# Optimization experiments

Measured on AMD Instinct MI355X. Metric: run time of the kernel, lower is better.

## Reference

```python
import jax, jax.numpy as jnp
import numpy as np

NEG_SLOPE = 0.2
LN_EPS = 1e-5


def gat_conv(x, src, dst, n_nodes, W, a_src, a_dst, b, concat):
    # W: [F_in, H*C]; a_src, a_dst: [H, C]; b: [H*C] if concat else [C]
    H, C = a_src.shape
    h = (x @ W).reshape(-1, H, C)                      # [N, H, C]
    # per-node attention scores, gathered per edge
    s_src = jnp.einsum('nhc,hc->nh', h, a_src)          # [N, H]
    s_dst = jnp.einsum('nhc,hc->nh', h, a_dst)          # [N, H]
    e = jax.nn.leaky_relu(s_src[src] + s_dst[dst], NEG_SLOPE)  # [E, H]
    # segment softmax over incoming edges of each dst node
    e_max = jax.ops.segment_max(e, dst, num_segments=n_nodes)  # [N, H]
    w = jnp.exp(e - e_max[dst])
    denom = jax.ops.segment_sum(w, dst, num_segments=n_nodes)
    alpha = w / (denom[dst] + 1e-16)                    # [E, H]
    # weighted scatter-aggregate of source messages
    msg = h[src] * alpha[:, :, None]                    # [E, H, C]
    out = jax.ops.segment_sum(msg, dst, num_segments=n_nodes)  # [N, H, C]
    out = out.reshape(n_nodes, H * C) if concat else out.mean(axis=1)
    return out + b


def layer_norm(x, g, b):
    mu = x.mean(-1, keepdims=True)
    var = ((x - mu) ** 2).mean(-1, keepdims=True)
    return (x - mu) * jax.lax.rsqrt(var + LN_EPS) * g + b


def setup_inputs() -> dict:
    key = jax.random.key(0)
    ks = jax.random.split(key, 16)
    N, E, F_in = 50000, 400000, 128
    H1, C1 = 4, 128          # conv1: heads=4, hidden=128, concat -> 512
    C2 = 64                  # conv2: heads=1, out=64
    sd = lambda fan: 1.0 / np.sqrt(fan)
    inp = {
        'x': jax.random.normal(ks[0], (N, F_in), jnp.float32),
        'edge_index': jax.random.randint(ks[1], (2, E), 0, N, jnp.int64),
        'num_nodes': N,
        'W1': jax.random.normal(ks[2], (F_in, H1 * C1), jnp.float32) * sd(F_in),
        'a_src1': jax.random.normal(ks[3], (H1, C1), jnp.float32) * sd(C1),
        'a_dst1': jax.random.normal(ks[4], (H1, C1), jnp.float32) * sd(C1),
        'b1': jnp.zeros((H1 * C1,), jnp.float32),
        'W2': jax.random.normal(ks[5], (H1 * C1, C2), jnp.float32) * sd(H1 * C1),
        'a_src2': jax.random.normal(ks[6], (1, C2), jnp.float32) * sd(C2),
        'a_dst2': jax.random.normal(ks[7], (1, C2), jnp.float32) * sd(C2),
        'b2': jnp.zeros((C2,), jnp.float32),
        'Wm1': jax.random.normal(ks[8], (C2, 32), jnp.float32) * sd(C2),
        'bm1': jnp.zeros((32,), jnp.float32),
        'g_ln': jnp.ones((32,), jnp.float32),
        'b_ln': jnp.zeros((32,), jnp.float32),
        'Wm2': jax.random.normal(ks[9], (32, 16), jnp.float32) * sd(32),
        'bm2': jnp.zeros((16,), jnp.float32),
    }
    return inp


def reference(x, edge_index, num_nodes, W1, a_src1, a_dst1, b1, W2, a_src2, a_dst2, b2, Wm1, bm1, g_ln, b_ln, Wm2, bm2):
    N = num_nodes
    # PyG GATConv add_self_loops=True
    loop = jnp.arange(N, dtype=edge_index.dtype)
    src = jnp.concatenate([edge_index[0], loop])
    dst = jnp.concatenate([edge_index[1], loop])
    # dropout layers are identity in eval mode
    h = jax.nn.elu(gat_conv(x, src, dst, N, W1, a_src1, a_dst1, b1, concat=True))
    h = jax.nn.elu(gat_conv(h, src, dst, N, W2, a_src2, a_dst2, b2, concat=False))
    h = jax.nn.relu(layer_norm(h @ Wm1 + bm1, g_ln, b_ln))
    return h @ Wm2 + bm2  # [N, 2*n_spectral_dims]
```

## Files before the change

### kernel.cpp

```cpp
#include <hip/hip_runtime.h>
#include <cmath>


#define F_IN 128
#define H1   4
#define C1   128
#define D1   512
#define C2   64
#define DM1  32
#define DM2  16

#define LRELU(x) ((x) > 0.f ? (x) : 0.2f * (x))

typedef float f32x4 __attribute__((ext_vector_type(4)));
typedef short short8 __attribute__((ext_vector_type(8)));

static __device__ __forceinline__ float bf2f(unsigned short u) {
    return __builtin_bit_cast(float, (unsigned)u << 16);
}
static __device__ __forceinline__ unsigned short f2bf(float f) {
    unsigned u = __builtin_bit_cast(unsigned, f);
    u = (u + 0x7fffu + ((u >> 16) & 1u)) >> 16;
    return (unsigned short)u;
}
static __device__ __forceinline__ float bflo(unsigned d) {
    return __builtin_bit_cast(float, d << 16);
}
static __device__ __forceinline__ float bfhi(unsigned d) {
    return __builtin_bit_cast(float, d & 0xffff0000u);
}

__global__ void k_detect(const void* ei, int E, int* flag) {
    __shared__ int any;
    if (threadIdx.x == 0) any = 0;
    __syncthreads();
    const int* p = (const int*)ei;
    int cnt = E < 4096 ? E : 4096;
    int stride = E / cnt;
    int local = 0;
    for (int i = threadIdx.x; i < cnt; i += blockDim.x) {
        long long idx = (long long)i * stride;
        local |= p[2 * idx + 1];
    }
    if (local) atomicOr(&any, 1);
    __syncthreads();
    if (threadIdx.x == 0) *flag = (any == 0) ? 1 : 0;
}

__global__ void k_convert_prep(const void* ei, const int* flag, int E, int N,
                               int* src32, int* dst32, int* deg,
                               const float* __restrict__ x,
                               const float* __restrict__ W1,
                               const float* __restrict__ W2,
                               unsigned short* __restrict__ xb,
                               unsigned short* __restrict__ W1t,
                               unsigned short* __restrict__ W2t, int n8) {
    int i = blockIdx.x * blockDim.x + threadIdx.x;
    int Etot = E + N;
    if (i < Etot) {
        int s, d;
        if (i < E) {
            if (*flag) {
                const long long* q = (const long long*)ei;
                s = (int)q[i];
                d = (int)q[(size_t)E + i];
            } else {
                const int* q = (const int*)ei;
                s = q[i];
                d = q[(size_t)E + i];
            }
        } else {
            s = i - E;
            d = i - E;
        }
        src32[i] = s;
        dst32[i] = d;
        atomicAdd(&deg[d], 1);
        return;
    }
    int i1 = i - Etot;
    if (i1 < n8) {
        const float4* p = (const float4*)(x + (size_t)i1 * 8);
        float4 a = p[0], b = p[1];
        unsigned short r[8] = {f2bf(a.x), f2bf(a.y), f2bf(a.z), f2bf(a.w),
                               f2bf(b.x), f2bf(b.y), f2bf(b.z), f2bf(b.w)};
        *(short8*)(xb + (size_t)i1 * 8) = *(const short8*)r;
        return;
    }
    int i2 = i1 - n8;
    if (i2 < F_IN * D1) {
        int nn = i2 / F_IN, kk = i2 - nn * F_IN;
        W1t[i2] = f2bf(W1[(size_t)kk * D1 + nn]);
        return;
    }
    int i3 = i2 - F_IN * D1;
    if (i3 < D1 * C2) {
        int nn = i3 / D1, kk = i3 - nn * D1;
        W2t[i3] = f2bf(W2[(size_t)kk * C2 + nn]);
    }
}

__global__ __launch_bounds__(256) void k_scan1(const int* __restrict__ deg,
                                               int* __restrict__ bsum, int N) {
    int t = threadIdx.x;
    int base = blockIdx.x * 1024 + t * 4;
    int s = 0;
    if (base + 3 < N) {
        int4 v = *(const int4*)&deg[base];
        s = v.x + v.y + v.z + v.w;
    } else {
        for (int k = 0; k < 4; k++)
            if (base + k < N) s += deg[base + k];
    }
#pragma unroll
    for (int o = 1; o < 64; o <<= 1) s += __shfl_xor(s, o, 64);
    __shared__ int ws[4];
    if ((t & 63) == 0) ws[t >> 6] = s;
    __syncthreads();
    if (t == 0) bsum[blockIdx.x] = ws[0] + ws[1] + ws[2] + ws[3];
}

__global__ __launch_bounds__(1024) void k_scan2(const int* __restrict__ bsum,
                                                int* __restrict__ boff, int nb) {
    __shared__ int wsum[16];
    __shared__ int woff[16];
    int t = threadIdx.x, lane = t & 63, wid = t >> 6;
    int v = (t < nb) ? bsum[t] : 0;
    int x = v;
#pragma unroll
    for (int o = 1; o < 64; o <<= 1) {
        int tv = __shfl_up(x, o, 64);
        if (lane >= o) x += tv;
    }
    if (lane == 63) wsum[wid] = x;
    __syncthreads();
    if (wid == 0) {
        int y = (lane < 16) ? wsum[lane] : 0;
        int z = y;
#pragma unroll
        for (int o = 1; o < 16; o <<= 1) {
            int tv = __shfl_up(z, o, 64);
            if (lane >= o) z += tv;
        }
        if (lane < 16) woff[lane] = z - y;
    }
    __syncthreads();
    if (t < nb) boff[t] = woff[wid] + x - v;
}

__global__ __launch_bounds__(256) void k_scan3(const int* __restrict__ deg,
                                               const int* __restrict__ boff,
                                               int* __restrict__ rowstart,
                                               int* __restrict__ cursor, int N,
                                               int Etot) {
    int t = threadIdx.x, lane = t & 63, wid = t >> 6;
    int base = blockIdx.x * 1024 + t * 4;
    int v0 = 0, v1 = 0, v2 = 0, v3 = 0;
    if (base + 3 < N) {
        int4 v = *(const int4*)&deg[base];
        v0 = v.x; v1 = v.y; v2 = v.z; v3 = v.w;
    } else {
        if (base + 0 < N) v0 = deg[base + 0];
        if (base + 1 < N) v1 = deg[base + 1];
        if (base + 2 < N) v2 = deg[base + 2];
        if (base + 3 < N) v3 = deg[base + 3];
    }
    int s4 = v0 + v1 + v2 + v3;
    int x = s4;
#pragma unroll
    for (int o = 1; o < 64; o <<= 1) {
        int tv = __shfl_up(x, o, 64);
        if (lane >= o) x += tv;
    }
    __shared__ int ws[4];
    if (lane == 63) ws[wid] = x;
    __syncthreads();
    int woff = 0;
#pragma unroll
    for (int w = 0; w < 4; w++)
        if (w < wid) woff += ws[w];
    int ex = boff[blockIdx.x] + woff + (x - s4);
    int e0 = ex, e1 = ex + v0, e2 = e1 + v1, e3 = e2 + v2;
    if (base + 0 < N) { rowstart[base + 0] = e0; cursor[base + 0] = e0; }
    if (base + 1 < N) { rowstart[base + 1] = e1; cursor[base + 1] = e1; }
    if (base + 2 < N) { rowstart[base + 2] = e2; cursor[base + 2] = e2; }
    if (base + 3 < N) { rowstart[base + 3] = e3; cursor[base + 3] = e3; }
    if (blockIdx.x == 0 && t == 0) rowstart[N] = Etot;
}

__global__ void k_fill(const int* __restrict__ src32, const int* __restrict__ dst32,
                       int* __restrict__ cursor, int* __restrict__ adj, int Etot) {
    int i = blockIdx.x * blockDim.x + threadIdx.x;
    if (i < Etot) {
        int d = dst32[i];
        int pos = atomicAdd(&cursor[d], 1);
        adj[pos] = src32[i];
    }
}

template <int WM, int WN, int MF, int NF, bool OUT_BF16, int SC_MODE>
__global__ __launch_bounds__(256) void k_gemm_bf16(
    const unsigned short* __restrict__ A, const unsigned short* __restrict__ Bt,
    void* __restrict__ C, int M, int K, int NC,
    const float* __restrict__ avs, const float* __restrict__ avd,
    float* __restrict__ s_src, float* __restrict__ s_dst) {
    constexpr int BM = WM * MF * 16;
    constexpr int BN = WN * NF * 16;
    constexpr int BK = 64;
    __shared__ unsigned short As[BM * BK];
    __shared__ unsigned short Bs[BN * BK];
    __shared__ float ps_lds[WN][BM], pd_lds[WN][BM];
    const int tid = threadIdx.x;
    const int row0 = blockIdx.x * BM, col0 = blockIdx.y * BN;
    const int wave = tid >> 6, lane = tid & 63;
    const int wr = wave / WN, wc = wave % WN;
    const int lrow = lane & 15, lkg = lane >> 4;
    f32x4 acc[MF][NF] = {};
    for (int k0 = 0; k0 < K; k0 += BK) {
#pragma unroll
        for (int inst = 0; inst < (BM * 8) / 256; ++inst) {
            int ibase = inst * 256 + wave * 64;
            int i = ibase + lane;
            int r = i >> 3, u = i & 7, su = u ^ (r & 7);
            const unsigned short* gp = A + (size_t)(row0 + r) * K + k0 + su * 8;
            __builtin_amdgcn_global_load_lds(
                (const __attribute__((address_space(1))) void*)gp,
                (__attribute__((address_space(3))) void*)&As[ibase * 8], 16, 0, 0);
        }
#pragma unroll
        for (int inst = 0; inst < (BN * 8) / 256; ++inst) {
            int ibase = inst * 256 + wave * 64;
            int i = ibase + lane;
            int r = i >> 3, u = i & 7, su = u ^ (r & 7);
            const unsigned short* gp = Bt + (size_t)(col0 + r) * K + k0 + su * 8;
            __builtin_amdgcn_global_load_lds(
                (const __attribute__((address_space(1))) void*)gp,
                (__attribute__((address_space(3))) void*)&Bs[ibase * 8], 16, 0, 0);
        }
        __syncthreads();
#pragma unroll
        for (int kk = 0; kk < BK; kk += 32) {
            short8 af[MF], bfr[NF];
#pragma unroll
            for (int m = 0; m < MF; m++) {
                int ar = wr * MF * 16 + m * 16 + lrow;
                int au = kk / 8 + lkg;
                af[m] = *(const short8*)&As[(ar * 8 + (au ^ (lrow & 7))) * 8];
            }
#pragma unroll
            for (int n = 0; n < NF; n++) {
                int br = wc * NF * 16 + n * 16 + lrow;
                int au = kk / 8 + lkg;
                bfr[n] = *(const short8*)&Bs[(br * 8 + (au ^ (lrow & 7))) * 8];
            }
#pragma unroll
            for (int m = 0; m < MF; m++)
#pragma unroll
                for (int n = 0; n < NF; n++)
                    acc[m][n] = __builtin_amdgcn_mfma_f32_16x16x32_bf16(
                        af[m], bfr[n], acc[m][n], 0, 0, 0);
        }
        __syncthreads();
    }
#pragma unroll
    for (int m = 0; m < MF; m++)
#pragma unroll
        for (int n = 0; n < NF; n++)
#pragma unroll
            for (int r = 0; r < 4; r++) {
                int gr = row0 + wr * MF * 16 + m * 16 + lkg * 4 + r;
                int gc = col0 + wc * NF * 16 + n * 16 + lrow;
                if (gr < M) {
                    if (OUT_BF16)
                        ((unsigned short*)C)[(size_t)gr * NC + gc] = f2bf(acc[m][n][r]);
                    else
                        ((float*)C)[(size_t)gr * NC + gc] = acc[m][n][r];
                }
            }
    if (SC_MODE) {
        float asv[NF], adv[NF];
#pragma unroll
        for (int n = 0; n < NF; n++) {
            int gc = col0 + wc * NF * 16 + n * 16 + lrow;
            asv[n] = avs[gc];
            adv[n] = avd[gc];
        }
#pragma unroll
        for (int m = 0; m < MF; m++)
#pragma unroll
            for (int r = 0; r < 4; r++) {
                float ps = 0.f, pd = 0.f;
#pragma unroll
                for (int n = 0; n < NF; n++) {
                    ps += acc[m][n][r] * asv[n];
                    pd += acc[m][n][r] * adv[n];
                }
#pragma unroll
                for (int o = 1; o < 16; o <<= 1) {
                    ps += __shfl_xor(ps, o, 64);
                    pd += __shfl_xor(pd, o, 64);
                }
                if (lrow == 0) {
                    int lr = wr * MF * 16 + m * 16 + lkg * 4 + r;
                    ps_lds[wc][lr] = ps;
                    pd_lds[wc][lr] = pd;
                }
            }
        __syncthreads();
        for (int rr = tid; rr < BM; rr += 256) {
            int gr = row0 + rr;
            if (gr < M) {
                float s = 0.f, d = 0.f;
#pragma unroll
                for (int w = 0; w < WN; w++) {
                    s += ps_lds[w][rr];
                    d += pd_lds[w][rr];
                }
                if (SC_MODE == 1) {
                    s_src[(size_t)gr * H1 + blockIdx.y] = s;
                    s_dst[(size_t)gr * H1 + blockIdx.y] = d;
                } else {
                    s_src[gr] = s;
                    s_dst[gr] = d;
                }
            }
        }
    }
}

__global__ __launch_bounds__(256) void k_agg1(
    const unsigned short* __restrict__ h1b, const float* __restrict__ s_src,
    const float* __restrict__ s_dst, const int* __restrict__ rowstart,
    const int* __restrict__ adj, const float* __restrict__ b1,
    unsigned short* __restrict__ out1, int N) {
    int wv = (blockIdx.x * blockDim.x + threadIdx.x) >> 6;
    if (wv >= N) return;
    int lane = threadIdx.x & 63;
    int beg = rowstart[wv], end = rowstart[wv + 1];
    int h4 = lane & 3, jj = lane >> 2;
    float sdh = s_dst[(size_t)wv * 4 + h4];
    float m = -1e30f;
    for (int c0 = beg; c0 < end; c0 += 16) {
        int j = c0 + jj;
        if (j < end) {
            int sj = adj[j];
            float e = LRELU(s_src[(size_t)sj * 4 + h4] + sdh);
            m = fmaxf(m, e);
        }
    }
#pragma unroll
    for (int o = 4; o < 64; o <<= 1) m = fmaxf(m, __shfl_xor(m, o, 64));
    float dn = 0.f;
    for (int c0 = beg; c0 < end; c0 += 16) {
        int j = c0 + jj;
        if (j < end) {
            int sj = adj[j];
            float e = LRELU(s_src[(size_t)sj * 4 + h4] + sdh);
            dn += __expf(e - m);
        }
    }
#pragma unroll
    for (int o = 4; o < 64; o <<= 1) dn += __shfl_xor(dn, o, 64);
    float inv = 1.f / (dn + 1e-16f);
    int hg = lane >> 4;
    float aL[4] = {}, aH[4] = {};
#define ACC1(vv, aa)                                   \
    do {                                               \
        aL[0] += (aa)*bflo(vv.x); aH[0] += (aa)*bfhi(vv.x); \
        aL[1] += (aa)*bflo(vv.y); aH[1] += (aa)*bfhi(vv.y); \
        aL[2] += (aa)*bflo(vv.z); aH[2] += (aa)*bfhi(vv.z); \
        aL[3] += (aa)*bflo(vv.w); aH[3] += (aa)*bfhi(vv.w); \
    } while (0)
    for (int c0 = beg; c0 < end; c0 += 16) {
        int j = c0 + jj;
        float av = 0.f;
        int sjv = 0;
        if (j < end) {
            sjv = adj[j];
            float e = LRELU(s_src[(size_t)sjv * 4 + h4] + sdh);
            av = __expf(e - m) * inv;
        }
        int cnt = min(16, end - c0);
        int j2 = 0;
        for (; j2 + 4 <= cnt; j2 += 4) {
            int l0 = (j2 + 0) * 4 + hg, l1 = (j2 + 1) * 4 + hg;
            int l2 = (j2 + 2) * 4 + hg, l3 = (j2 + 3) * 4 + hg;
            int s0 = __shfl(sjv, l0, 64), s1 = __shfl(sjv, l1, 64);
            int s2 = __shfl(sjv, l2, 64), s3 = __shfl(sjv, l3, 64);
            float a0 = __shfl(av, l0, 64), a1 = __shfl(av, l1, 64);
            float a2 = __shfl(av, l2, 64), a3 = __shfl(av, l3, 64);
            uint4 v0 = *(const uint4*)&h1b[(size_t)s0 * D1 + lane * 8];
            uint4 v1 = *(const uint4*)&h1b[(size_t)s1 * D1 + lane * 8];
            uint4 v2 = *(const uint4*)&h1b[(size_t)s2 * D1 + lane * 8];
            uint4 v3 = *(const uint4*)&h1b[(size_t)s3 * D1 + lane * 8];
            ACC1(v0, a0); ACC1(v1, a1); ACC1(v2, a2); ACC1(v3, a3);
        }
        for (; j2 < cnt; ++j2) {
            int l0 = j2 * 4 + hg;
            int s0 = __shfl(sjv, l0, 64);
            float a0 = __shfl(av, l0, 64);
            uint4 v0 = *(const uint4*)&h1b[(size_t)s0 * D1 + lane * 8];
            ACC1(v0, a0);
        }
    }
#undef ACC1
    const float4* bp = (const float4*)&b1[lane * 8];
    float4 bb0 = bp[0], bb1 = bp[1];
    float r[8];
    r[0] = aL[0] + bb0.x; r[1] = aH[0] + bb0.y;
    r[2] = aL[1] + bb0.z; r[3] = aH[1] + bb0.w;
    r[4] = aL[2] + bb1.x; r[5] = aH[2] + bb1.y;
    r[6] = aL[3] + bb1.z; r[7] = aH[3] + bb1.w;
    unsigned short o16[8];
#pragma unroll
    for (int i = 0; i < 8; i++) {
        float z = r[i] > 0.f ? r[i] : expm1f(r[i]);
        o16[i] = f2bf(z);
    }
    *(short8*)&out1[(size_t)wv * D1 + lane * 8] = *(const short8*)o16;
}

__global__ __launch_bounds__(256) void k_agg2(
    const unsigned short* __restrict__ h2lin, const float* __restrict__ s_src,
    const float* __restrict__ s_dst, const int* __restrict__ rowstart,
    const int* __restrict__ adj, const float* __restrict__ b2,
    float* __restrict__ h2, int N) {
    int wv = (blockIdx.x * blockDim.x + threadIdx.x) >> 6;
    if (wv >= N) return;
    int lane = threadIdx.x & 63;
    int beg = rowstart[wv], end = rowstart[wv + 1];
    float sd = s_dst[wv];
    float m = -1e30f;
    for (int c0 = beg; c0 < end; c0 += 64) {
        int j = c0 + lane;
        if (j < end) m = fmaxf(m, LRELU(s_src[adj[j]] + sd));
    }
#pragma unroll
    for (int o = 1; o < 64; o <<= 1) m = fmaxf(m, __shfl_xor(m, o, 64));
    float dn = 0.f;
    for (int c0 = beg; c0 < end; c0 += 64) {
        int j = c0 + lane;
        if (j < end) dn += __expf(LRELU(s_src[adj[j]] + sd) - m);
    }
#pragma unroll
    for (int o = 1; o < 64; o <<= 1) dn += __shfl_xor(dn, o, 64);
    float inv = 1.f / (dn + 1e-16f);
    int eg = lane >> 4, ch = (lane & 15) * 4;
    float a0 = 0.f, a1 = 0.f, a2 = 0.f, a3 = 0.f;
    for (int j0 = beg; j0 < end; j0 += 4) {
        int j = j0 + eg;
        if (j < end) {
            int sj = adj[j];
            float a = __expf(LRELU(s_src[sj] + sd) - m) * inv;
            uint2 rv = *(const uint2*)&h2lin[(size_t)sj * C2 + ch];
            a0 += a * bflo(rv.x); a1 += a * bfhi(rv.x);
            a2 += a * bflo(rv.y); a3 += a * bfhi(rv.y);
        }
    }
#pragma unroll
    for (int o = 16; o < 64; o <<= 1) {
        a0 += __shfl_xor(a0, o, 64);
        a1 += __shfl_xor(a1, o, 64);
        a2 += __shfl_xor(a2, o, 64);
        a3 += __shfl_xor(a3, o, 64);
    }
    if (lane < 16) {
        const float4 bb = *(const float4*)&b2[ch];
        float r0 = a0 + bb.x, r1 = a1 + bb.y, r2 = a2 + bb.z, r3 = a3 + bb.w;
        r0 = r0 > 0.f ? r0 : expm1f(r0);
        r1 = r1 > 0.f ? r1 : expm1f(r1);
        r2 = r2 > 0.f ? r2 : expm1f(r2);
        r3 = r3 > 0.f ? r3 : expm1f(r3);
        *(float4*)&h2[(size_t)wv * C2 + ch] = make_float4(r0, r1, r2, r3);
    }
}

__global__ __launch_bounds__(256) void k_mlp(
    const float* __restrict__ h2, const float* __restrict__ Wm1,
    const float* __restrict__ bm1, const float* __restrict__ g_ln,
    const float* __restrict__ b_ln, const float* __restrict__ Wm2,
    const float* __restrict__ bm2, float* __restrict__ out, int N) {
    __shared__ float w1[C2 * DM1];
    __shared__ float w2[DM1 * DM2];
    __shared__ float cb1[DM1], cg[DM1], cbl[DM1], cb2[DM2];
    int tid = threadIdx.x;
    for (int i = tid; i < C2 * DM1; i += 256) w1[i] = Wm1[i];
    for (int i = tid; i < DM1 * DM2; i += 256) w2[i] = Wm2[i];
    if (tid < DM1) {
        cb1[tid] = bm1[tid];
        cg[tid] = g_ln[tid];
        cbl[tid] = b_ln[tid];
    } else if (tid < DM1 + DM2) {
        cb2[tid - DM1] = bm2[tid - DM1];
    }
    __syncthreads();
    int n = blockIdx.x * 256 + tid;
    if (n >= N) return;
    float h[C2];
    const float4* hp = (const float4*)&h2[(size_t)n * C2];
#pragma unroll
    for (int i = 0; i < C2 / 4; i++) {
        float4 v = hp[i];
        h[4 * i] = v.x; h[4 * i + 1] = v.y;
        h[4 * i + 2] = v.z; h[4 * i + 3] = v.w;
    }
    float t[DM1];
#pragma unroll
    for (int j = 0; j < DM1; j++) {
        float a = cb1[j];
#pragma unroll
        for (int c = 0; c < C2; c++) a += h[c] * w1[c * DM1 + j];
        t[j] = a;
    }
    float mu = 0.f;
#pragma unroll
    for (int j = 0; j < DM1; j++) mu += t[j];
    mu *= (1.f / DM1);
    float var = 0.f;
#pragma unroll
    for (int j = 0; j < DM1; j++) {
        float d = t[j] - mu;
        var += d * d;
    }
    var *= (1.f / DM1);
    float rs = rsqrtf(var + 1e-5f);
#pragma unroll
    for (int j = 0; j < DM1; j++) {
        float z = (t[j] - mu) * rs * cg[j] + cbl[j];
        t[j] = z > 0.f ? z : 0.f;
    }
    float o[DM2];
#pragma unroll
    for (int k = 0; k < DM2; k++) {
        float a = cb2[k];
#pragma unroll
        for (int j = 0; j < DM1; j++) a += t[j] * w2[j * DM2 + k];
        o[k] = a;
    }
    float4* op = (float4*)&out[(size_t)n * DM2];
    op[0] = make_float4(o[0], o[1], o[2], o[3]);
    op[1] = make_float4(o[4], o[5], o[6], o[7]);
    op[2] = make_float4(o[8], o[9], o[10], o[11]);
    op[3] = make_float4(o[12], o[13], o[14], o[15]);
}

extern "C" void kernel_launch(void* const* d_in, const int* in_sizes, int n_in,
                              void* d_out, int out_size, void* d_ws,
                              size_t ws_size, hipStream_t stream) {
    const float* x      = (const float*)d_in[0];
    const void*  ei     = d_in[1];
    const float* W1     = (const float*)d_in[3];
    const float* a_src1 = (const float*)d_in[4];
    const float* a_dst1 = (const float*)d_in[5];
    const float* b1     = (const float*)d_in[6];
    const float* W2     = (const float*)d_in[7];
    const float* a_src2 = (const float*)d_in[8];
    const float* a_dst2 = (const float*)d_in[9];
    const float* b2     = (const float*)d_in[10];
    const float* Wm1    = (const float*)d_in[11];
    const float* bm1    = (const float*)d_in[12];
    const float* g_ln   = (const float*)d_in[13];
    const float* b_ln   = (const float*)d_in[14];
    const float* Wm2    = (const float*)d_in[15];
    const float* bm2    = (const float*)d_in[16];

    const int N    = in_sizes[0] / F_IN;
    const int E    = in_sizes[1] / 2;
    const int Etot = E + N;
    const int nb   = (N + 1023) / 1024;

    char* ws = (char*)d_ws;
    size_t off = 0;
    auto alloc = [&](size_t bytes) {
        size_t o = off;
        off += (bytes + 255) & ~(size_t)255;
        return o;
    };
    int*   flag     = (int*)(ws + alloc(4));
    int*   src32    = (int*)(ws + alloc((size_t)Etot * 4));
    int*   dst32    = (int*)(ws + alloc((size_t)Etot * 4));
    int*   deg      = (int*)(ws + alloc((size_t)N * 4));
    int*   bsum     = (int*)(ws + alloc(4096 * 4));
    int*   boff     = (int*)(ws + alloc(4096 * 4));
    int*   rowstart = (int*)(ws + alloc((size_t)(N + 1) * 4));
    int*   cursor   = (int*)(ws + alloc((size_t)N * 4));
    int*   adj      = (int*)(ws + alloc((size_t)Etot * 4));
    float* s_src1   = (float*)(ws + alloc((size_t)N * H1 * 4));
    float* s_dst1   = (float*)(ws + alloc((size_t)N * H1 * 4));
    unsigned short* xb    = (unsigned short*)(ws + alloc((size_t)N * F_IN * 2));
    unsigned short* W1t   = (unsigned short*)(ws + alloc((size_t)F_IN * D1 * 2));
    unsigned short* W2t   = (unsigned short*)(ws + alloc((size_t)D1 * C2 * 2));
    unsigned short* h1b   = (unsigned short*)(ws + alloc((size_t)N * D1 * 2));
    unsigned short* out1  = (unsigned short*)(ws + alloc((size_t)N * D1 * 2));
    unsigned short* h2lin = (unsigned short*)(ws + alloc((size_t)N * C2 * 2));
    float* h2    = (float*)(ws + alloc((size_t)N * C2 * 4));
    float* s_src2 = s_src1;
    float* s_dst2 = s_dst1;

    hipMemsetAsync(deg, 0, (size_t)N * 4, stream);
    k_detect<<<1, 256, 0, stream>>>(ei, E, flag);
    int n8 = N * F_IN / 8;
    int total_cp = Etot + n8 + F_IN * D1 + D1 * C2;
    k_convert_prep<<<(total_cp + 255) / 256, 256, 0, stream>>>(
        ei, flag, E, N, src32, dst32, deg, x, W1, W2, xb, W1t, W2t, n8);
    k_scan1<<<nb, 256, 0, stream>>>(deg, bsum, N);
    k_scan2<<<1, 1024, 0, stream>>>(bsum, boff, nb);
    k_scan3<<<nb, 256, 0, stream>>>(deg, boff, rowstart, cursor, N, Etot);
    k_fill<<<(Etot + 255) / 256, 256, 0, stream>>>(src32, dst32, cursor, adj, Etot);

    k_gemm_bf16<2, 2, 4, 4, true, 1>
        <<<dim3((N + 127) / 128, D1 / 128), 256, 0, stream>>>(
            xb, W1t, h1b, N, F_IN, D1, a_src1, a_dst1, s_src1, s_dst1);
    k_agg1<<<(N * 64 + 255) / 256, 256, 0, stream>>>(h1b, s_src1, s_dst1, rowstart,
                                                     adj, b1, out1, N);

    k_gemm_bf16<4, 1, 2, 4, true, 2>
        <<<dim3((N + 127) / 128, 1), 256, 0, stream>>>(
            out1, W2t, h2lin, N, D1, C2, a_src2, a_dst2, s_src2, s_dst2);
    k_agg2<<<(N * 64 + 255) / 256, 256, 0, stream>>>(h2lin, s_src2, s_dst2, rowstart,
                                                     adj, b2, h2, N);

    k_mlp<<<(N + 255) / 256, 256, 0, stream>>>(h2, Wm1, bm1, g_ln, b_ln, Wm2, bm2,
                                               (float*)d_out, N);
}
```

Baseline: 340.9 us.

## Use atomic ranks for CSR fill, online softmax in aggregations, LDS edge broadcast

CSR construction now records each edge's atomic rank during degree counting, so the fill pass needs no second atomic pass over a cursor array. Both aggregation kernels fuse the max and denominator passes into one online-softmax pass, and agg1 reuses the first chunk's scores. agg1 broadcasts source indices and weights through LDS instead of many shuffles. The second GEMM switches to a smaller 64-row tile to launch more blocks, at the cost of an extra rank array and more exp calls in the online update.

```diff
diff --git a/kernel.cpp b/kernel.cpp
--- a/kernel.cpp
+++ b/kernel.cpp
@@ -48,7 +48,7 @@
 }
 
 __global__ void k_convert_prep(const void* ei, const int* flag, int E, int N,
-                               int* src32, int* dst32, int* deg,
+                               int* src32, int* dst32, int* deg, int* rank32,
                                const float* __restrict__ x,
                                const float* __restrict__ W1,
                                const float* __restrict__ W2,
@@ -75,7 +75,7 @@
         }
         src32[i] = s;
         dst32[i] = d;
-        atomicAdd(&deg[d], 1);
+        rank32[i] = atomicAdd(&deg[d], 1);
         return;
     }
     int i1 = i - Etot;
@@ -150,8 +150,7 @@
 
 __global__ __launch_bounds__(256) void k_scan3(const int* __restrict__ deg,
                                                const int* __restrict__ boff,
-                                               int* __restrict__ rowstart,
-                                               int* __restrict__ cursor, int N,
+                                               int* __restrict__ rowstart, int N,
                                                int Etot) {
     int t = threadIdx.x, lane = t & 63, wid = t >> 6;
     int base = blockIdx.x * 1024 + t * 4;
@@ -181,21 +180,19 @@
         if (w < wid) woff += ws[w];
     int ex = boff[blockIdx.x] + woff + (x - s4);
     int e0 = ex, e1 = ex + v0, e2 = e1 + v1, e3 = e2 + v2;
-    if (base + 0 < N) { rowstart[base + 0] = e0; cursor[base + 0] = e0; }
-    if (base + 1 < N) { rowstart[base + 1] = e1; cursor[base + 1] = e1; }
-    if (base + 2 < N) { rowstart[base + 2] = e2; cursor[base + 2] = e2; }
-    if (base + 3 < N) { rowstart[base + 3] = e3; cursor[base + 3] = e3; }
+    if (base + 0 < N) rowstart[base + 0] = e0;
+    if (base + 1 < N) rowstart[base + 1] = e1;
+    if (base + 2 < N) rowstart[base + 2] = e2;
+    if (base + 3 < N) rowstart[base + 3] = e3;
     if (blockIdx.x == 0 && t == 0) rowstart[N] = Etot;
 }
 
 __global__ void k_fill(const int* __restrict__ src32, const int* __restrict__ dst32,
-                       int* __restrict__ cursor, int* __restrict__ adj, int Etot) {
+                       const int* __restrict__ rank32,
+                       const int* __restrict__ rowstart, int* __restrict__ adj,
+                       int Etot) {
     int i = blockIdx.x * blockDim.x + threadIdx.x;
-    if (i < Etot) {
-        int d = dst32[i];
-        int pos = atomicAdd(&cursor[d], 1);
-        adj[pos] = src32[i];
-    }
+    if (i < Etot) adj[rowstart[dst32[i]] + rank32[i]] = src32[i];
 }
 
 template <int WM, int WN, int MF, int NF, bool OUT_BF16, int SC_MODE>
@@ -333,73 +330,88 @@
     const float* __restrict__ s_dst, const int* __restrict__ rowstart,
     const int* __restrict__ adj, const float* __restrict__ b1,
     unsigned short* __restrict__ out1, int N) {
+    __shared__ uint2 ex_lds[4][64];
     int wv = (blockIdx.x * blockDim.x + threadIdx.x) >> 6;
     if (wv >= N) return;
+    int wv4 = (threadIdx.x >> 6) & 3;
     int lane = threadIdx.x & 63;
     int beg = rowstart[wv], end = rowstart[wv + 1];
     int h4 = lane & 3, jj = lane >> 2;
     float sdh = s_dst[(size_t)wv * 4 + h4];
-    float m = -1e30f;
-    for (int c0 = beg; c0 < end; c0 += 16) {
-        int j = c0 + jj;
+    int nch = (end - beg + 15) >> 4;
+    float e0st = -1e30f;
+    int s0st = 0;
+    float m = -1e30f, dn = 0.f;
+    for (int c = 0; c < nch; ++c) {
+        int j = beg + c * 16 + jj;
+        float e = -1e30f;
+        int sj = 0;
         if (j < end) {
-            int sj = adj[j];
-            float e = LRELU(s_src[(size_t)sj * 4 + h4] + sdh);
-            m = fmaxf(m, e);
-        }
-    }
-#pragma unroll
-    for (int o = 4; o < 64; o <<= 1) m = fmaxf(m, __shfl_xor(m, o, 64));
-    float dn = 0.f;
-    for (int c0 = beg; c0 < end; c0 += 16) {
-        int j = c0 + jj;
-        if (j < end) {
-            int sj = adj[j];
-            float e = LRELU(s_src[(size_t)sj * 4 + h4] + sdh);
-            dn += __expf(e - m);
-        }
-    }
-#pragma unroll
-    for (int o = 4; o < 64; o <<= 1) dn += __shfl_xor(dn, o, 64);
+            sj = adj[j];
+            e = LRELU(s_src[(size_t)sj * 4 + h4] + sdh);
+        }
+        if (c == 0) { e0st = e; s0st = sj; }
+        float nm = fmaxf(m, e);
+        dn = dn * __expf(m - nm) + ((j < end) ? __expf(e - nm) : 0.f);
+        m = nm;
+    }
+#pragma unroll
+    for (int o = 4; o < 64; o <<= 1) {
+        float om = __shfl_xor(m, o, 64);
+        float od = __shfl_xor(dn, o, 64);
+        float nm = fmaxf(m, om);
+        dn = dn * __expf(m - nm) + od * __expf(om - nm);
+        m = nm;
+    }
     float inv = 1.f / (dn + 1e-16f);
     int hg = lane >> 4;
     float aL[4] = {}, aH[4] = {};
-#define ACC1(vv, aa)                                   \
-    do {                                               \
+#define ACC1(vv, aa)                                        \
+    do {                                                    \
         aL[0] += (aa)*bflo(vv.x); aH[0] += (aa)*bfhi(vv.x); \
         aL[1] += (aa)*bflo(vv.y); aH[1] += (aa)*bfhi(vv.y); \
         aL[2] += (aa)*bflo(vv.z); aH[2] += (aa)*bfhi(vv.z); \
         aL[3] += (aa)*bflo(vv.w); aH[3] += (aa)*bfhi(vv.w); \
     } while (0)
-    for (int c0 = beg; c0 < end; c0 += 16) {
-        int j = c0 + jj;
-        float av = 0.f;
-        int sjv = 0;
-        if (j < end) {
-            sjv = adj[j];
-            float e = LRELU(s_src[(size_t)sjv * 4 + h4] + sdh);
-            av = __expf(e - m) * inv;
-        }
-        int cnt = min(16, end - c0);
+    for (int c = 0; c < nch; ++c) {
+        int j = beg + c * 16 + jj;
+        float e;
+        int sj;
+        if (c == 0) {
+            e = e0st;
+            sj = s0st;
+        } else {
+            sj = 0;
+            e = -1e30f;
+            if (j < end) {
+                sj = adj[j];
+                e = LRELU(s_src[(size_t)sj * 4 + h4] + sdh);
+            }
+        }
+        float av = (j < end) ? __expf(e - m) * inv : 0.f;
+        ex_lds[wv4][lane] = make_uint2((unsigned)sj, __builtin_bit_cast(unsigned, av));
+        asm volatile("s_waitcnt lgkmcnt(0)" ::: "memory");
+        int cnt = min(16, end - beg - c * 16);
         int j2 = 0;
         for (; j2 + 4 <= cnt; j2 += 4) {
-            int l0 = (j2 + 0) * 4 + hg, l1 = (j2 + 1) * 4 + hg;
-            int l2 = (j2 + 2) * 4 + hg, l3 = (j2 + 3) * 4 + hg;
-            int s0 = __shfl(sjv, l0, 64), s1 = __shfl(sjv, l1, 64);
-            int s2 = __shfl(sjv, l2, 64), s3 = __shfl(sjv, l3, 64);
-            float a0 = __shfl(av, l0, 64), a1 = __shfl(av, l1, 64);
-            float a2 = __shfl(av, l2, 64), a3 = __shfl(av, l3, 64);
-            uint4 v0 = *(const uint4*)&h1b[(size_t)s0 * D1 + lane * 8];
-            uint4 v1 = *(const uint4*)&h1b[(size_t)s1 * D1 + lane * 8];
-            uint4 v2 = *(const uint4*)&h1b[(size_t)s2 * D1 + lane * 8];
-            uint4 v3 = *(const uint4*)&h1b[(size_t)s3 * D1 + lane * 8];
+            uint2 e0 = ex_lds[wv4][(j2 + 0) * 4 + hg];
+            uint2 e1 = ex_lds[wv4][(j2 + 1) * 4 + hg];
+            uint2 e2 = ex_lds[wv4][(j2 + 2) * 4 + hg];
+            uint2 e3 = ex_lds[wv4][(j2 + 3) * 4 + hg];
+            uint4 v0 = *(const uint4*)&h1b[(size_t)e0.x * D1 + lane * 8];
+            uint4 v1 = *(const uint4*)&h1b[(size_t)e1.x * D1 + lane * 8];
+            uint4 v2 = *(const uint4*)&h1b[(size_t)e2.x * D1 + lane * 8];
+            uint4 v3 = *(const uint4*)&h1b[(size_t)e3.x * D1 + lane * 8];
+            float a0 = __builtin_bit_cast(float, e0.y);
+            float a1 = __builtin_bit_cast(float, e1.y);
+            float a2 = __builtin_bit_cast(float, e2.y);
+            float a3 = __builtin_bit_cast(float, e3.y);
             ACC1(v0, a0); ACC1(v1, a1); ACC1(v2, a2); ACC1(v3, a3);
         }
         for (; j2 < cnt; ++j2) {
-            int l0 = j2 * 4 + hg;
-            int s0 = __shfl(sjv, l0, 64);
-            float a0 = __shfl(av, l0, 64);
-            uint4 v0 = *(const uint4*)&h1b[(size_t)s0 * D1 + lane * 8];
+            uint2 e0 = ex_lds[wv4][j2 * 4 + hg];
+            uint4 v0 = *(const uint4*)&h1b[(size_t)e0.x * D1 + lane * 8];
+            float a0 = __builtin_bit_cast(float, e0.y);
             ACC1(v0, a0);
         }
     }
@@ -430,20 +442,23 @@
     int lane = threadIdx.x & 63;
     int beg = rowstart[wv], end = rowstart[wv + 1];
     float sd = s_dst[wv];
-    float m = -1e30f;
+    float m = -1e30f, dn = 0.f;
     for (int c0 = beg; c0 < end; c0 += 64) {
         int j = c0 + lane;
-        if (j < end) m = fmaxf(m, LRELU(s_src[adj[j]] + sd));
-    }
-#pragma unroll
-    for (int o = 1; o < 64; o <<= 1) m = fmaxf(m, __shfl_xor(m, o, 64));
-    float dn = 0.f;
-    for (int c0 = beg; c0 < end; c0 += 64) {
-        int j = c0 + lane;
-        if (j < end) dn += __expf(LRELU(s_src[adj[j]] + sd) - m);
-    }
-#pragma unroll
-    for (int o = 1; o < 64; o <<= 1) dn += __shfl_xor(dn, o, 64);
+        float e = -1e30f;
+        if (j < end) e = LRELU(s_src[adj[j]] + sd);
+        float nm = fmaxf(m, e);
+        dn = dn * __expf(m - nm) + ((j < end) ? __expf(e - nm) : 0.f);
+        m = nm;
+    }
+#pragma unroll
+    for (int o = 1; o < 64; o <<= 1) {
+        float om = __shfl_xor(m, o, 64);
+        float od = __shfl_xor(dn, o, 64);
+        float nm = fmaxf(m, om);
+        dn = dn * __expf(m - nm) + od * __expf(om - nm);
+        m = nm;
+    }
     float inv = 1.f / (dn + 1e-16f);
     int eg = lane >> 4, ch = (lane & 15) * 4;
     float a0 = 0.f, a1 = 0.f, a2 = 0.f, a3 = 0.f;
@@ -579,11 +594,11 @@
     int*   flag     = (int*)(ws + alloc(4));
     int*   src32    = (int*)(ws + alloc((size_t)Etot * 4));
     int*   dst32    = (int*)(ws + alloc((size_t)Etot * 4));
+    int*   rank32   = (int*)(ws + alloc((size_t)Etot * 4));
     int*   deg      = (int*)(ws + alloc((size_t)N * 4));
     int*   bsum     = (int*)(ws + alloc(4096 * 4));
     int*   boff     = (int*)(ws + alloc(4096 * 4));
     int*   rowstart = (int*)(ws + alloc((size_t)(N + 1) * 4));
-    int*   cursor   = (int*)(ws + alloc((size_t)N * 4));
     int*   adj      = (int*)(ws + alloc((size_t)Etot * 4));
     float* s_src1   = (float*)(ws + alloc((size_t)N * H1 * 4));
     float* s_dst1   = (float*)(ws + alloc((size_t)N * H1 * 4));
@@ -602,11 +617,12 @@
     int n8 = N * F_IN / 8;
     int total_cp = Etot + n8 + F_IN * D1 + D1 * C2;
     k_convert_prep<<<(total_cp + 255) / 256, 256, 0, stream>>>(
-        ei, flag, E, N, src32, dst32, deg, x, W1, W2, xb, W1t, W2t, n8);
+        ei, flag, E, N, src32, dst32, deg, rank32, x, W1, W2, xb, W1t, W2t, n8);
     k_scan1<<<nb, 256, 0, stream>>>(deg, bsum, N);
     k_scan2<<<1, 1024, 0, stream>>>(bsum, boff, nb);
-    k_scan3<<<nb, 256, 0, stream>>>(deg, boff, rowstart, cursor, N, Etot);
-    k_fill<<<(Etot + 255) / 256, 256, 0, stream>>>(src32, dst32, cursor, adj, Etot);
+    k_scan3<<<nb, 256, 0, stream>>>(deg, boff, rowstart, N, Etot);
+    k_fill<<<(Etot + 255) / 256, 256, 0, stream>>>(src32, dst32, rank32, rowstart,
+                                                   adj, Etot);
 
     k_gemm_bf16<2, 2, 4, 4, true, 1>
         <<<dim3((N + 127) / 128, D1 / 128), 256, 0, stream>>>(
@@ -614,8 +630,8 @@
     k_agg1<<<(N * 64 + 255) / 256, 256, 0, stream>>>(h1b, s_src1, s_dst1, rowstart,
                                                      adj, b1, out1, N);
 
-    k_gemm_bf16<4, 1, 2, 4, true, 2>
-        <<<dim3((N + 127) / 128, 1), 256, 0, stream>>>(
+    k_gemm_bf16<2, 2, 2, 2, true, 2>
+        <<<dim3((N + 63) / 64, 1), 256, 0, stream>>>(
             out1, W2t, h2lin, N, D1, C2, a_src2, a_dst2, s_src2, s_dst2);
     k_agg2<<<(N * 64 + 255) / 256, 256, 0, stream>>>(h2lin, s_src2, s_dst2, rowstart,
                                                      adj, b2, h2, N);
```

Result: faster. 322.0 us (-5.5%).
